# Kernel optimization log

Measured on AMD Instinct MI355X. Metric: run time of the kernel, lower is better.

Reference implementation:

```python
import jax, jax.numpy as jnp
from jax import lax
import numpy as np


def conv2d(x, w, b=None, stride=1, padding=0, groups=1, dilation=1):
    out = lax.conv_general_dilated(
        x, w, (stride, stride), [(padding, padding)] * 2,
        rhs_dilation=(dilation, dilation), feature_group_count=groups,
        dimension_numbers=('NCHW', 'OIHW', 'NCHW'))
    return out if b is None else out + b[None, :, None, None]


def unfold1d(x, k, axis):
    # torch.nn.functional.unfold with kernel (k,1) or (1,k), pad k//2 on that axis.
    # Returns [B, C, k, H, W] (channel-major, kernel-tap inner), matching torch layout.
    pad = k // 2
    pads = [(0, 0)] * 4
    pads[axis] = (pad, pad)
    xp = jnp.pad(x, pads)
    return jnp.stack([lax.slice_in_dim(xp, i, i + x.shape[axis], axis=axis)
                      for i in range(k)], axis=2)


def ikba(x, att, k, g, b_cb, w_cb):
    # Per-pixel dynamic grouped conv: attention mixes nset codebook kernels,
    # applied as vertical (k,1) then horizontal (1,k) unfold-matmul-fold.
    B, c, H, W = x.shape
    nset = att.shape[1]
    cg = c // g
    P = H * W
    a = att.reshape(B, nset, P).transpose(0, 2, 1)          # [B,P,nset]
    bias = a @ b_cb[0]                                      # [B,P,c]
    attk = a @ w_cb[0]                                      # [B,P, 2*c*cg*k]
    half = attk.shape[-1] // 2
    ah = attk[..., :half].reshape(B, P, g, cg, cg * k)
    aw = attk[..., half:].reshape(B, P, g, cg, cg * k)
    # vertical pass
    ufh = unfold1d(x, k, 2).reshape(B, g, cg * k, P).transpose(0, 3, 1, 2)  # [B,P,g,cg*k]
    xh = jnp.einsum('bpgij,bpgj->bpgi', ah, ufh).reshape(B, P, c)
    xh = xh.transpose(0, 2, 1).reshape(B, c, H, W)
    # horizontal pass
    ufw = unfold1d(xh, k, 3).reshape(B, g, cg * k, P).transpose(0, 3, 1, 2)
    xw = jnp.einsum('bpgij,bpgj->bpgi', aw, ufw).reshape(B, P, c) + bias
    return xw.transpose(0, 2, 1).reshape(B, c, H, W)


def hff_forward(x, dw1_w, dw2_w, proj_w, lka0_w, lkas_w, lka1_w, lka1_b,
                sca_w, sca_b, c1a_w, c1b_w, c2a_w, c2a_b, c2b_w, c2b_b,
                c211_w, c211_b, w_cb, b_cb, attgamma, ga1):
    C = x.shape[1]
    K, GC = 3, 4
    g = C // GC
    sca = conv2d(jnp.mean(x, axis=(2, 3), keepdims=True), sca_w, sca_b)
    x1 = conv2d(conv2d(x, dw1_w), dw2_w, padding=1, groups=C)
    lka = conv2d(conv2d(conv2d(x, lka0_w, padding=2, groups=C),
                        lkas_w, padding=9, groups=C, dilation=3), lka1_w, lka1_b)
    t = conv2d(x, c2a_w, c2a_b, padding=1, groups=c2a_w.shape[0])
    t1, t2 = jnp.split(t, 2, axis=1)  # SimpleGate
    att = conv2d(t1 * t2, c2b_w, c2b_b) * attgamma + conv2d(x, c211_w, c211_b)
    uf = conv2d(conv2d(x, c1a_w), c1b_w, padding=1, groups=C)
    x2 = ikba(uf, att, K, g, b_cb, w_cb) * ga1 + uf
    return conv2d(x1 * x2 * sca * lka, proj_w)


def setup_inputs() -> dict:
    key = jax.random.key(0)
    ks = jax.random.split(key, 24)
    B, C, H, W = 2, 256, 64, 64
    nset, k, gc = 128, 3, 4
    g = C // gc
    cg = C // g
    def rn(i, shape, scale=0.02):
        return jax.random.normal(ks[i], shape, jnp.float32) * scale
    return {
        'x': jax.random.normal(ks[0], (B, C, H, W), jnp.float32),
        'dw1_w': rn(1, (C, C, 1, 1)),
        'dw2_w': rn(2, (C, 1, 3, 3), 0.1),
        'proj_w': rn(3, (C, C, 1, 1)),
        'lka0_w': rn(4, (C, 1, 5, 5), 0.1),
        'lkas_w': rn(5, (C, 1, 7, 7), 0.1),
        'lka1_w': rn(6, (C, C, 1, 1)),
        'lka1_b': rn(7, (C,)),
        'sca_w': rn(8, (C, C, 1, 1)),
        'sca_b': rn(9, (C,)),
        'c1a_w': rn(10, (C, C, 1, 1)),
        'c1b_w': rn(11, (C, 1, 3, 3), 0.1),
        'c2a_w': rn(12, (32, C // 32, 3, 3), 0.1),
        'c2a_b': rn(13, (32,)),
        'c2b_w': rn(14, (nset, 16, 1, 1), 0.1),
        'c2b_b': rn(15, (nset,)),
        'c211_w': rn(16, (nset, C, 1, 1)),
        'c211_b': rn(17, (nset,)),
        'w_cb': rn(18, (1, nset, C * cg * k * 2), 0.05),
        'b_cb': rn(19, (1, nset, C), 0.05),
        'attgamma': jnp.full((1, nset, 1, 1), 0.01, jnp.float32),
        'ga1': jnp.full((1, C, 1, 1), 0.01, jnp.float32),
    }


def reference(x, dw1_w, dw2_w, proj_w, lka0_w, lkas_w, lka1_w, lka1_b,
              sca_w, sca_b, c1a_w, c1b_w, c2a_w, c2a_b, c2b_w, c2b_b,
              c211_w, c211_b, w_cb, b_cb, attgamma, ga1):
    return hff_forward(x, dw1_w, dw2_w, proj_w, lka0_w, lkas_w, lka1_w, lka1_b,
                       sca_w, sca_b, c1a_w, c1b_w, c2a_w, c2a_b, c2b_w, c2b_b,
                       c211_w, c211_b, w_cb, b_cb, attgamma, ga1)
```

## Files before the change

### kernel.cpp

```cpp
#include <hip/hip_runtime.h>
#include <cstddef>

#define P_ 4096
#define HW_ 64

typedef __bf16 bf16x8 __attribute__((ext_vector_type(8)));
typedef float f32x4 __attribute__((ext_vector_type(4)));

__device__ inline ushort f2bf(float f) {
  unsigned u = __float_as_uint(f);
  unsigned r = (u + 0x7FFFu + ((u >> 16) & 1u)) >> 16;
  return (ushort)r;
}
__device__ inline float bf2f(ushort h) {
  return __uint_as_float(((unsigned)h) << 16);
}
__device__ inline unsigned pack2(ushort a, ushort b) {
  return (unsigned)a | ((unsigned)b << 16);
}


__device__ inline void xsplit_body(const float* sb, ushort* dhb, ushort* dlb,
                                   int p0, int K, char* smem) {
  float (*T)[65] = (float(*)[65])smem;
  int t = threadIdx.x;
#pragma unroll
  for (int i = 0; i < 32; ++i) {
    int l = i * 256 + t;
    int n = l >> 6, c = l & 63;
    T[n][c] = sb[(size_t)n * P_ + p0 + c];
  }
  __syncthreads();
#pragma unroll
  for (int i = 0; i < 4; ++i) {
    int l = i * 256 + t;
    int c = l >> 4, n8 = (l & 15) << 3;
    ushort vh[8], vl[8];
#pragma unroll
    for (int u = 0; u < 8; ++u) {
      float f = T[n8 + u][c];
      ushort h = f2bf(f);
      vh[u] = h;
      vl[u] = f2bf(f - bf2f(h));
    }
    *(uint4*)&dhb[(size_t)(p0 + c) * K + n8] = *(uint4*)vh;
    *(uint4*)&dlb[(size_t)(p0 + c) * K + n8] = *(uint4*)vl;
  }
}

__device__ inline void gemm_body(const ushort* Whb, const ushort* Wlb,
                                 const ushort* Xhb, const ushort* Xlb,
                                 const float* bias, float* out, int M, int m0,
                                 int p0, int b, int K, char* smem) {
  ushort* Wsh = (ushort*)smem;
  ushort* Wsl = (ushort*)(smem + 9216);
  ushort* Xsh = (ushort*)(smem + 18432);
  ushort* Xsl = (ushort*)(smem + 27648);
  int t = threadIdx.x;
  int w = t >> 6, lane = t & 63, lm = lane & 15, lq = lane >> 4;
  f32x4 C[4];
#pragma unroll
  for (int pt = 0; pt < 4; ++pt) C[pt] = (f32x4)(0.f);
  for (int k0 = 0; k0 < K; k0 += 64) {
#pragma unroll
    for (int i = 0; i < 2; ++i) {
      int u = i * 256 + t;
      int row = u >> 3, k8 = (u & 7) * 8;
      *(uint4*)&Wsh[row * 72 + k8] = *(const uint4*)&Whb[(size_t)row * K + k0 + k8];
      *(uint4*)&Wsl[row * 72 + k8] = *(const uint4*)&Wlb[(size_t)row * K + k0 + k8];
      *(uint4*)&Xsh[row * 72 + k8] = *(const uint4*)&Xhb[(size_t)row * K + k0 + k8];
      *(uint4*)&Xsl[row * 72 + k8] = *(const uint4*)&Xlb[(size_t)row * K + k0 + k8];
    }
    __syncthreads();
#pragma unroll
    for (int kt = 0; kt < 2; ++kt) {
      bf16x8 Ah = *(const bf16x8*)&Wsh[(w * 16 + lm) * 72 + kt * 32 + lq * 8];
      bf16x8 Al = *(const bf16x8*)&Wsl[(w * 16 + lm) * 72 + kt * 32 + lq * 8];
#pragma unroll
      for (int pt = 0; pt < 4; ++pt) {
        bf16x8 Bh = *(const bf16x8*)&Xsh[(pt * 16 + lm) * 72 + kt * 32 + lq * 8];
        bf16x8 Bl = *(const bf16x8*)&Xsl[(pt * 16 + lm) * 72 + kt * 32 + lq * 8];
        C[pt] = __builtin_amdgcn_mfma_f32_16x16x32_bf16(Ah, Bh, C[pt], 0, 0, 0);
        C[pt] = __builtin_amdgcn_mfma_f32_16x16x32_bf16(Al, Bh, C[pt], 0, 0, 0);
        C[pt] = __builtin_amdgcn_mfma_f32_16x16x32_bf16(Ah, Bl, C[pt], 0, 0, 0);
      }
    }
    __syncthreads();
  }
#pragma unroll
  for (int pt = 0; pt < 4; ++pt) {
    int p = p0 + pt * 16 + lm;
#pragma unroll
    for (int r = 0; r < 4; ++r) {
      int m = m0 + w * 16 + lq * 4 + r;
      float v = C[pt][r];
      if (bias) v += bias[m];
      out[((size_t)b * M + m) * P_ + p] = v;
    }
  }
}

__global__ __launch_bounds__(256) void prep_kernel(
    const float* __restrict__ w_cb, const float* __restrict__ dw1_w,
    const float* __restrict__ lka1_w, const float* __restrict__ c1a_w,
    const float* __restrict__ proj_w, const float* __restrict__ c211_w,
    const float* __restrict__ b_cb, ushort* __restrict__ wT,
    ushort* __restrict__ W5h, ushort* __restrict__ W5l,
    ushort* __restrict__ bth, ushort* __restrict__ btl,
    const float* __restrict__ x, float* __restrict__ mean,
    ushort* __restrict__ XTxh, ushort* __restrict__ XTxl,
    const float* __restrict__ w0, const float* __restrict__ w1,
    float* __restrict__ outlka) {
  __shared__ __align__(16) char smem[48448];
  float (*T)[65] = (float(*)[65])smem;
  int blk = blockIdx.x;
  int t = threadIdx.x;
  if (blk < 512) {
    float* p0a = (float*)smem;
    float* p1a = (float*)(smem + 19584);
    int bc = blk;
    const float* ib = x + (size_t)bc * P_;
    const float* wp0 = w0 + (size_t)(bc & 255) * 25;
    const float* wp1 = w1 + (size_t)(bc & 255) * 49;
    for (int i = t; i < 4896; i += 256) p0a[i] = 0.f;
    for (int i = t; i < 7216; i += 256) p1a[i] = 0.f;
    __syncthreads();
#pragma unroll
    for (int i = 0; i < 4; ++i) {
      int l = i * 1024 + t * 4;
      int y = l >> 6, xx = l & 63;
      *(float4*)&p0a[(y + 2) * 72 + 4 + xx] = *(const float4*)(ib + l);
    }
    __syncthreads();
    int x0 = (t & 15) * 4, y0 = (t >> 4) * 4;
    {
      float acc[4][4] = {};
#pragma unroll
      for (int ry = 0; ry < 8; ++ry) {
        const float* row = &p0a[(y0 + ry) * 72 + x0];
        float4 v0 = *(const float4*)row;
        float4 v1 = *(const float4*)(row + 4);
        float4 v2 = *(const float4*)(row + 8);
        float rv[12] = {v0.x, v0.y, v0.z, v0.w, v1.x, v1.y, v1.z, v1.w,
                        v2.x, v2.y, v2.z, v2.w};
#pragma unroll
        for (int oy = 0; oy < 4; ++oy) {
          int dy = ry - oy;
          if (dy >= 0 && dy <= 4) {
#pragma unroll
            for (int dx = 0; dx < 5; ++dx) {
              float wv = wp0[dy * 5 + dx];
#pragma unroll
              for (int ox = 0; ox < 4; ++ox)
                acc[oy][ox] += wv * rv[2 + ox + dx];
            }
          }
        }
      }
#pragma unroll
      for (int oy = 0; oy < 4; ++oy) {
        float4 v = {acc[oy][0], acc[oy][1], acc[oy][2], acc[oy][3]};
        *(float4*)&p1a[(y0 + oy + 9) * 88 + 12 + x0] = v;
      }
    }
    __syncthreads();
    {
      float acc[4][4] = {};
#pragma unroll
      for (int ry = 0; ry < 22; ++ry) {
        const float* row = &p1a[(y0 + ry) * 88 + x0];
        float rv[28];
#pragma unroll
        for (int q = 0; q < 7; ++q)
          *(float4*)&rv[q * 4] = *(const float4*)(row + q * 4);
#pragma unroll
        for (int oy = 0; oy < 4; ++oy) {
          int d = ry - oy;
          if (d >= 0 && d <= 18 && (d % 3) == 0) {
            int dy = d / 3;
#pragma unroll
            for (int dx = 0; dx < 7; ++dx) {
              float wv = wp1[dy * 7 + dx];
#pragma unroll
              for (int ox = 0; ox < 4; ++ox)
                acc[oy][ox] += wv * rv[3 + ox + 3 * dx];
            }
          }
        }
      }
      float* ob = outlka + (size_t)bc * P_;
#pragma unroll
      for (int oy = 0; oy < 4; ++oy) {
        float4 v = {acc[oy][0], acc[oy][1], acc[oy][2], acc[oy][3]};
        *(float4*)&ob[(y0 + oy) * 64 + x0] = v;
      }
    }
  } else if (blk < 608) {
    int c0 = (blk - 512) * 64;
#pragma unroll
    for (int i = 0; i < 32; ++i) {
      int l = i * 256 + t;
      int n = l >> 6, c = l & 63;
      T[n][c] = w_cb[(size_t)n * 6144 + c0 + c];
    }
    __syncthreads();
#pragma unroll
    for (int i = 0; i < 4; ++i) {
      int l = i * 256 + t;
      int c = l >> 4, n8 = (l & 15) << 3;
      ushort v[8];
#pragma unroll
      for (int u = 0; u < 8; ++u) v[u] = f2bf(T[n8 + u][c]);
      *(uint4*)&wT[(size_t)(c0 + c) * 128 + n8] = *(uint4*)v;
    }
  } else if (blk < 752) {
    int f = (blk - 608) * 2048 + t * 8;
    const float* srcs[5] = {dw1_w, lka1_w, c1a_w, proj_w, c211_w};
    const int base[6] = {0, 65536, 131072, 196608, 262144, 294912};
    int r = 0;
    while (f >= base[r + 1]) ++r;
    const float* s = srcs[r] + (f - base[r]);
    float4 a = *(const float4*)s;
    float4 b4 = *(const float4*)(s + 4);
    float vv[8] = {a.x, a.y, a.z, a.w, b4.x, b4.y, b4.z, b4.w};
    ushort vh[8], vl[8];
#pragma unroll
    for (int u = 0; u < 8; ++u) {
      ushort h = f2bf(vv[u]);
      vh[u] = h;
      vl[u] = f2bf(vv[u] - bf2f(h));
    }
    *(uint4*)&W5h[f] = *(uint4*)vh;
    *(uint4*)&W5l[f] = *(uint4*)vl;
  } else if (blk < 756) {
    int c0 = (blk - 752) * 64;
#pragma unroll
    for (int i = 0; i < 32; ++i) {
      int l = i * 256 + t;
      int n = l >> 6, c = l & 63;
      T[n][c] = b_cb[(size_t)n * 256 + c0 + c];
    }
    __syncthreads();
#pragma unroll
    for (int i = 0; i < 4; ++i) {
      int l = i * 256 + t;
      int c = l >> 4, n8 = (l & 15) << 3;
      ushort vh[8], vl[8];
#pragma unroll
      for (int u = 0; u < 8; ++u) {
        float fv = T[n8 + u][c];
        ushort h = f2bf(fv);
        vh[u] = h;
        vl[u] = f2bf(fv - bf2f(h));
      }
      *(uint4*)&bth[(size_t)(c0 + c) * 128 + n8] = *(uint4*)vh;
      *(uint4*)&btl[(size_t)(c0 + c) * 128 + n8] = *(uint4*)vl;
    }
  } else if (blk < 1268) {
    int bc = blk - 756;
    const float* xp = x + (size_t)bc * P_;
    float s = 0.f;
    for (int i = t; i < P_; i += 256) s += xp[i];
    float* red = (float*)smem;
    red[t] = s;
    __syncthreads();
    for (int off2 = 128; off2 > 0; off2 >>= 1) {
      if (t < off2) red[t] += red[t + off2];
      __syncthreads();
    }
    if (t == 0) mean[bc] = red[0] * (1.f / P_);
  } else {
    const int K = 256;
    int l = blk - 1268;
    int p0 = (l & 63) * 64;
    int kb = (l >> 6) & 1;
    int b = l >> 7;
    xsplit_body(x + ((size_t)b * K + kb * 128) * P_,
                XTxh + (size_t)b * P_ * K + (size_t)kb * 128,
                XTxl + (size_t)b * P_ * K + (size_t)kb * 128, p0, K, smem);
  }
}

__global__ __launch_bounds__(256) void main1_kernel(
    const ushort* __restrict__ Xh, const ushort* __restrict__ Xl,
    const ushort* __restrict__ W5h, const ushort* __restrict__ W5l,
    const float* __restrict__ c211_b, float* __restrict__ dw1_out,
    float* __restrict__ B3, float* __restrict__ att0,
    const float* __restrict__ x, const float* __restrict__ c2aw,
    const float* __restrict__ c2ab, float* __restrict__ sgate,
    const float* __restrict__ B6, ushort* __restrict__ XT2h,
    ushort* __restrict__ XT2l, const float* __restrict__ mean,
    const float* __restrict__ sca_w, const float* __restrict__ sca_b,
    float* __restrict__ sca) {
  __shared__ __align__(16) char smem[36864];
  int blk = blockIdx.x;
  int t = threadIdx.x;
  if (blk < 1280) {
    const int K = 256;
    int p = blk & 63;
    int my = (blk >> 6) % 10;
    int b = blk / 640;
    const ushort *Wh, *Wl;
    float* out;
    const float* bias = nullptr;
    int M, m0;
    if (my < 4) {
      Wh = W5h; Wl = W5l; out = dw1_out; M = 256; m0 = my * 64;
    } else if (my < 8) {
      Wh = W5h + 131072; Wl = W5l + 131072; out = B3; M = 256; m0 = (my - 4) * 64;
    } else {
      Wh = W5h + 262144; Wl = W5l + 262144; out = att0; M = 128;
      m0 = (my - 8) * 64; bias = c211_b;
    }
    int p0 = p * 64;
    gemm_body(Wh + (size_t)m0 * K, Wl + (size_t)m0 * K,
              Xh + ((size_t)b * P_ + p0) * K, Xl + ((size_t)b * P_ + p0) * K,
              bias, out, M, m0, p0, b, K, smem);
  } else if (blk < 1792) {
    int idx = (blk - 1280) * 256 + t;
    int xq = idx & 63, y = (idx >> 6) & 63, go = (idx >> 12) & 15, b = idx >> 16;
    float acc[2];
#pragma unroll
    for (int h = 0; h < 2; ++h) {
      int gc = go + h * 16;
      const float* wr = c2aw + gc * 72;
      const float* xb = x + ((size_t)b * 256 + gc * 8) * P_;
      float ss = c2ab[gc];
      for (int ci = 0; ci < 8; ++ci)
        for (int dy = 0; dy < 3; ++dy) {
          int yy = y + dy - 1;
          if (yy < 0 || yy >= 64) continue;
          for (int dx = 0; dx < 3; ++dx) {
            int xx = xq + dx - 1;
            if (xx < 0 || xx >= 64) continue;
            ss += wr[ci * 9 + dy * 3 + dx] * xb[(size_t)ci * P_ + yy * 64 + xx];
          }
        }
      acc[h] = ss;
    }
    sgate[idx] = acc[0] * acc[1];
  } else if (blk < 2048) {
    const int K = 256;
    int l = blk - 1792;
    int p0 = (l & 63) * 64;
    int kb = (l >> 6) & 1;
    int b = l >> 7;
    xsplit_body(B6 + ((size_t)b * K + kb * 128) * P_,
                XT2h + (size_t)b * P_ * K + (size_t)kb * 128,
                XT2l + (size_t)b * P_ * K + (size_t)kb * 128, p0, K, smem);
  } else {
    int b = blk - 2048, c = t;
    const float* mb = mean + b * 256;
    const float* wr = sca_w + c * 256;
    float s = sca_b[c];
    for (int k = 0; k < 256; ++k) s += wr[k] * mb[k];
    sca[b * 256 + c] = s;
  }
}

__global__ __launch_bounds__(256) void k3_kernel(
    const ushort* __restrict__ Wh, const ushort* __restrict__ Wl,
    const ushort* __restrict__ XT2h, const ushort* __restrict__ XT2l,
    const float* __restrict__ lka1_b, float* __restrict__ B1,
    const float* __restrict__ sb, const float* __restrict__ c2bw,
    const float* __restrict__ c2bb, const float* __restrict__ gamma,
    const float* __restrict__ res, ushort* __restrict__ outh,
    ushort* __restrict__ outl, const float* __restrict__ in1,
    const float* __restrict__ w1, float* __restrict__ out1,
    const float* __restrict__ in2, const float* __restrict__ w2,
    float* __restrict__ out2) {
  __shared__ __align__(16) char smem[36864];
  int blk = blockIdx.x;
  int t = threadIdx.x;
  if (blk < 512) {
    const int K = 256;
    int p0 = (blk & 63) * 64;
    int m0 = ((blk >> 6) & 3) * 64;
    int b = blk >> 8;
    gemm_body(Wh + (size_t)m0 * K, Wl + (size_t)m0 * K,
              XT2h + ((size_t)b * P_ + p0) * K, XT2l + ((size_t)b * P_ + p0) * K,
              lka1_b, B1, 256, m0, p0, b, K, smem);
  } else if (blk < 768) {
    const int K = 16, M = 128;
    int l = blk - 512;
    int p0 = (l & 63) * 64;
    int m0 = ((l >> 6) & 1) * 64;
    int b = l >> 7;
    float (*Ws)[68] = (float(*)[68])smem;
    float (*Xs)[68] = (float(*)[68])(smem + 4352 * 4);
    int tm = t >> 4, tp = t & 15;
    float acc[4][4] = {};
    const float* inb = sb + (size_t)b * K * P_;
    {
      int kk = t >> 4, pq = (t & 15) << 2;
      float4 v = *(const float4*)(inb + (size_t)kk * P_ + p0 + pq);
      *(float4*)&Xs[kk][pq] = v;
    }
    {
      int mm = t >> 2, kq = (t & 3) << 2;
      float4 v = *(const float4*)(c2bw + (size_t)(m0 + mm) * K + kq);
      Ws[kq + 0][mm] = v.x; Ws[kq + 1][mm] = v.y;
      Ws[kq + 2][mm] = v.z; Ws[kq + 3][mm] = v.w;
    }
    __syncthreads();
#pragma unroll
    for (int kk = 0; kk < 16; ++kk) {
      const float4 wv = *(const float4*)&Ws[kk][tm << 2];
      const float4 xv = *(const float4*)&Xs[kk][tp << 2];
      const float wa[4] = {wv.x, wv.y, wv.z, wv.w};
      const float xa[4] = {xv.x, xv.y, xv.z, xv.w};
#pragma unroll
      for (int i = 0; i < 4; ++i)
#pragma unroll
        for (int j = 0; j < 4; ++j) acc[i][j] += wa[i] * xa[j];
    }
    float val[4][4];
#pragma unroll
    for (int i = 0; i < 4; ++i) {
      int m = m0 + (tm << 2) + i;
      float bv = c2bb[m], gm = gamma[m];
      float4 rv = *(const float4*)(res + ((size_t)b * M + m) * P_ + p0 + (tp << 2));
      val[i][0] = (acc[i][0] + bv) * gm + rv.x;
      val[i][1] = (acc[i][1] + bv) * gm + rv.y;
      val[i][2] = (acc[i][2] + bv) * gm + rv.z;
      val[i][3] = (acc[i][3] + bv) * gm + rv.w;
    }
#pragma unroll
    for (int j = 0; j < 4; ++j) {
      int p = p0 + (tp << 2) + j;
      ushort vh[4], vl[4];
#pragma unroll
      for (int i = 0; i < 4; ++i) {
        float f = val[i][j];
        ushort h = f2bf(f);
        vh[i] = h;
        vl[i] = f2bf(f - bf2f(h));
      }
      size_t a = ((size_t)b * P_ + p) * 128 + m0 + (tm << 2);
      uint2 hv, lv;
      hv.x = pack2(vh[0], vh[1]); hv.y = pack2(vh[2], vh[3]);
      lv.x = pack2(vl[0], vl[1]); lv.y = pack2(vl[2], vl[3]);
      *(uint2*)&outh[a] = hv;
      *(uint2*)&outl[a] = lv;
    }
  } else {
    float* pl = (float*)smem;
    int l = blk - 768;
    int which = l >> 9;
    int bc = l & 511;
    const float* in = which ? in2 : in1;
    const float* w = which ? w2 : w1;
    float* out = which ? out2 : out1;
    const float* ib = in + (size_t)bc * P_;
    const float* wp = w + (size_t)(bc & 255) * 9;
    for (int i = t; i < 4752; i += 256) pl[i] = 0.f;
    __syncthreads();
#pragma unroll
    for (int i = 0; i < 4; ++i) {
      int ll = i * 1024 + t * 4;
      int y = ll >> 6, xx = ll & 63;
      *(float4*)&pl[(y + 1) * 72 + 4 + xx] = *(const float4*)(ib + ll);
    }
    __syncthreads();
    int x0 = (t & 15) * 4, y0 = (t >> 4) * 4;
    float acc[4][4] = {};
#pragma unroll
    for (int ry = 0; ry < 6; ++ry) {
      const float* row = &pl[(y0 + ry) * 72 + x0];
      float4 v0 = *(const float4*)row;
      float4 v1 = *(const float4*)(row + 4);
      float4 v2 = *(const float4*)(row + 8);
      float rv[12] = {v0.x, v0.y, v0.z, v0.w, v1.x, v1.y, v1.z, v1.w,
                      v2.x, v2.y, v2.z, v2.w};
#pragma unroll
      for (int oy = 0; oy < 4; ++oy) {
        int dy = ry - oy;
        if (dy >= 0 && dy <= 2) {
#pragma unroll
          for (int dx = 0; dx < 3; ++dx) {
            float wv = wp[dy * 3 + dx];
#pragma unroll
            for (int ox = 0; ox < 4; ++ox)
              acc[oy][ox] += wv * rv[3 + ox + dx];
          }
        }
      }
    }
    float* ob = out + (size_t)bc * P_;
#pragma unroll
    for (int oy = 0; oy < 4; ++oy) {
      float4 v = {acc[oy][0], acc[oy][1], acc[oy][2], acc[oy][3]};
      *(float4*)&ob[(y0 + oy) * 64 + x0] = v;
    }
  }
}

__global__ __launch_bounds__(256) void ikba_mfma_kernel(
    const float* __restrict__ in, const ushort* __restrict__ attT,
    const ushort* __restrict__ Wt, int dirH, int wofs,
    const ushort* __restrict__ bth, const ushort* __restrict__ btl,
    const float* __restrict__ uf_ep, const float* __restrict__ ga1,
    const float* __restrict__ x1, const float* __restrict__ lka,
    const float* __restrict__ sca, ushort* __restrict__ pXh,
    ushort* __restrict__ pXl, float* __restrict__ outV) {
  __shared__ float Ts[4][64][17];

  int t = threadIdx.x;
  int b = blockIdx.z;
  int quad = blockIdx.y;
  int y = blockIdx.x;
  int p0 = y * 64;
  int gg = t >> 6;
  int lane = t & 63;
  int lm = lane & 15, lq = lane >> 4;
  int gi = quad * 4 + gg;
  int x = lane;
  float (*Tsw)[17] = Ts[gg];

  const ushort* Wbase = Wt + ((size_t)wofs + (size_t)gi * 48) * 128;
  bf16x8 Af[3][4];
#pragma unroll
  for (int ct = 0; ct < 3; ++ct)
#pragma unroll
    for (int K = 0; K < 4; ++K)
      Af[ct][K] = *(const bf16x8*)&Wbase[(ct * 16 + lm) * 128 + K * 32 + lq * 8];

  const ushort* Ab = attT + ((size_t)b * P_ + p0) * 128;
  f32x4 Cf[3][4];
#pragma unroll
  for (int ct = 0; ct < 3; ++ct)
#pragma unroll
    for (int pt = 0; pt < 4; ++pt) Cf[ct][pt] = (f32x4)(0.f);

#pragma unroll
  for (int pt = 0; pt < 4; ++pt) {
    bf16x8 Bf[4];
#pragma unroll
    for (int K = 0; K < 4; ++K)
      Bf[K] = *(const bf16x8*)&Ab[(pt * 16 + lm) * 128 + K * 32 + lq * 8];
#pragma unroll
    for (int ct = 0; ct < 3; ++ct)
#pragma unroll
      for (int K = 0; K < 4; ++K)
        Cf[ct][pt] = __builtin_amdgcn_mfma_f32_16x16x32_bf16(
            Af[ct][K], Bf[K], Cf[ct][pt], 0, 0, 0);
  }

  float u[12];
  const float* inb = in + ((size_t)b * 256 + gi * 4) * P_;
  if (dirH) {
#pragma unroll
    for (int j = 0; j < 12; ++j) {
      int ci = j / 3, tap = j % 3;
      int xx = x + tap - 1;
      u[j] = (xx >= 0 && xx < 64) ? inb[(size_t)ci * P_ + p0 + xx] : 0.f;
    }
  } else {
#pragma unroll
    for (int j = 0; j < 12; ++j) {
      int ci = j / 3, tap = j % 3;
      int yy = y + tap - 1;
      u[j] = (yy >= 0 && yy < 64) ? inb[(size_t)ci * P_ + yy * 64 + x] : 0.f;
    }
  }

  float s4[4] = {0.f, 0.f, 0.f, 0.f};
#pragma unroll
  for (int ct = 0; ct < 3; ++ct) {
#pragma unroll
    for (int pt = 0; pt < 4; ++pt)
#pragma unroll
      for (int r = 0; r < 4; ++r)
        Tsw[pt * 16 + lm][lq * 4 + r] = Cf[ct][pt][r];
    float tv[16];
#pragma unroll
    for (int c4 = 0; c4 < 4; ++c4)
      *(float4*)&tv[c4 * 4] = *(const float4*)&Tsw[x][c4 * 4];
#pragma unroll
    for (int c = 0; c < 16; ++c) {
      int col = ct * 16 + c;
      int i = col / 12, j = col % 12;
      s4[i] += tv[c] * u[j];
    }
  }

  if (dirH) {
    bf16x8 Abh[4], Abl[4];
#pragma unroll
    for (int K = 0; K < 4; ++K) {
      Abh[K] = *(const bf16x8*)&bth[(size_t)(quad * 16 + lm) * 128 + K * 32 + lq * 8];
      Abl[K] = *(const bf16x8*)&btl[(size_t)(quad * 16 + lm) * 128 + K * 32 + lq * 8];
    }
#pragma unroll
    for (int pt = 0; pt < 4; ++pt) {
      f32x4 Cb = (f32x4)(0.f);
#pragma unroll
      for (int K = 0; K < 4; ++K) {
        bf16x8 Bb = *(const bf16x8*)&Ab[(pt * 16 + lm) * 128 + K * 32 + lq * 8];
        Cb = __builtin_amdgcn_mfma_f32_16x16x32_bf16(Abh[K], Bb, Cb, 0, 0, 0);
        Cb = __builtin_amdgcn_mfma_f32_16x16x32_bf16(Abl[K], Bb, Cb, 0, 0, 0);
      }
#pragma unroll
      for (int r = 0; r < 4; ++r)
        Tsw[pt * 16 + lm][lq * 4 + r] = Cb[r];
    }
    float4 bl4 = *(const float4*)&Tsw[x][gg * 4];
    const float blv[4] = {bl4.x, bl4.y, bl4.z, bl4.w};
    ushort vh[4], vl[4];
#pragma unroll
    for (int i = 0; i < 4; ++i) {
      int ch = gi * 4 + i;
      size_t oidx = ((size_t)b * 256 + ch) * P_ + p0 + x;
      float x2v = (s4[i] + blv[i]) * ga1[ch] + uf_ep[oidx];
      float pr = x1[oidx] * x2v * sca[b * 256 + ch] * lka[oidx];
      ushort h = f2bf(pr);
      vh[i] = h;
      vl[i] = f2bf(pr - bf2f(h));
    }
    size_t xa = ((size_t)b * P_ + p0 + x) * 256 + quad * 16 + gg * 4;
    uint2 hv, lv;
    hv.x = pack2(vh[0], vh[1]); hv.y = pack2(vh[2], vh[3]);
    lv.x = pack2(vl[0], vl[1]); lv.y = pack2(vl[2], vl[3]);
    *(uint2*)&pXh[xa] = hv;
    *(uint2*)&pXl[xa] = lv;
  } else {
#pragma unroll
    for (int i = 0; i < 4; ++i) {
      int ch = gi * 4 + i;
      outV[((size_t)b * 256 + ch) * P_ + p0 + x] = s4[i];
    }
  }
}

__global__ __launch_bounds__(256) void gemm_bf16s_kernel(
    const ushort* __restrict__ Wh, const ushort* __restrict__ Wl,
    const ushort* __restrict__ Xh, const ushort* __restrict__ Xl,
    const float* __restrict__ bias, float* __restrict__ out, int M, int K) {
  __shared__ __align__(16) char smem[36864];
  int p0 = blockIdx.x * 64, m0 = blockIdx.y * 64, b = blockIdx.z;
  gemm_body(Wh + (size_t)m0 * K, Wl + (size_t)m0 * K,
            Xh + ((size_t)b * P_ + p0) * K, Xl + ((size_t)b * P_ + p0) * K,
            bias, out, M, m0, p0, b, K, smem);
}

extern "C" void kernel_launch(void* const* d_in, const int* in_sizes, int n_in,
                              void* d_out, int out_size, void* d_ws, size_t ws_size,
                              hipStream_t stream) {
  const float* x      = (const float*)d_in[0];
  const float* dw1_w  = (const float*)d_in[1];
  const float* dw2_w  = (const float*)d_in[2];
  const float* proj_w = (const float*)d_in[3];
  const float* lka0_w = (const float*)d_in[4];
  const float* lkas_w = (const float*)d_in[5];
  const float* lka1_w = (const float*)d_in[6];
  const float* lka1_b = (const float*)d_in[7];
  const float* sca_w  = (const float*)d_in[8];
  const float* sca_b  = (const float*)d_in[9];
  const float* c1a_w  = (const float*)d_in[10];
  const float* c1b_w  = (const float*)d_in[11];
  const float* c2a_w  = (const float*)d_in[12];
  const float* c2a_b  = (const float*)d_in[13];
  const float* c2b_w  = (const float*)d_in[14];
  const float* c2b_b  = (const float*)d_in[15];
  const float* c211_w = (const float*)d_in[16];
  const float* c211_b = (const float*)d_in[17];
  const float* w_cb   = (const float*)d_in[18];
  const float* b_cb   = (const float*)d_in[19];
  const float* attg   = (const float*)d_in[20];
  const float* ga1    = (const float*)d_in[21];
  float* out = (float*)d_out;

  const size_t NCHW = 2u * 256u * P_;
  float* ws = (float*)d_ws;
  size_t off = 0;
  float* meanb = ws + off; off += 512;
  float* scab  = ws + off; off += 512;
  float* B1 = ws + off; off += NCHW;
  float* B2 = ws + off; off += NCHW;
  float* B3 = ws + off; off += NCHW;
  float* B4 = ws + off; off += NCHW;
  float* B5 = ws + off; off += NCHW;
  float* B6 = ws + off; off += NCHW;
  float* sb   = ws + off; off += 2u * 16u * P_;
  float* att0 = ws + off; off += 2u * 128u * P_;
  ushort* wT    = (ushort*)(ws + off); off += 393216;
  ushort* W5h   = (ushort*)(ws + off); off += 147456;
  ushort* W5l   = (ushort*)(ws + off); off += 147456;
  ushort* bth   = (ushort*)(ws + off); off += 16384;
  ushort* btl   = (ushort*)(ws + off); off += 16384;
  ushort* XTxh  = (ushort*)(ws + off); off += 1048576;
  ushort* XTxl  = (ushort*)(ws + off); off += 1048576;
  ushort* XT2h  = (ushort*)(ws + off); off += 1048576;
  ushort* XT2l  = (ushort*)(ws + off); off += 1048576;
  ushort* XT3h  = (ushort*)(ws + off); off += 1048576;
  ushort* XT3l  = (ushort*)(ws + off); off += 1048576;
  ushort* attTh = (ushort*)(ws + off); off += 524288;
  ushort* attTl = (ushort*)(ws + off); off += 524288;

  const ushort* Wlka1h = W5h + 65536,  *Wlka1l = W5l + 65536;
  const ushort* Wprojh = W5h + 196608, *Wprojl = W5l + 196608;

  dim3 blk(256);

  prep_kernel<<<1524, blk, 0, stream>>>(w_cb, dw1_w, lka1_w, c1a_w, proj_w,
                                        c211_w, b_cb, wT, W5h, W5l, bth, btl,
                                        x, meanb, XTxh, XTxl,
                                        lka0_w, lkas_w, B6);
  main1_kernel<<<2050, blk, 0, stream>>>(XTxh, XTxl, W5h, W5l, c211_b,
                                         B4, B3, att0, x, c2a_w, c2a_b, sb,
                                         B6, XT2h, XT2l, meanb, sca_w, sca_b,
                                         scab);
  k3_kernel<<<1792, blk, 0, stream>>>(Wlka1h, Wlka1l, XT2h, XT2l, lka1_b, B1,
                                      sb, c2b_w, c2b_b, attg, att0,
                                      attTh, attTl,
                                      B4, dw2_w, B2, B3, c1b_w, B5);
  dim3 gik(64, 16, 2);
  ikba_mfma_kernel<<<gik, blk, 0, stream>>>(B5, attTh, wT, 0, 0, nullptr, nullptr,
                                            nullptr, nullptr, nullptr, nullptr,
                                            nullptr, nullptr, nullptr, B6);
  ikba_mfma_kernel<<<gik, blk, 0, stream>>>(B6, attTh, wT, 1, 3072, bth, btl,
                                            B5, ga1, B2, B1, scab, XT3h, XT3l,
                                            nullptr);
  gemm_bf16s_kernel<<<dim3(64, 4, 2), blk, 0, stream>>>(Wprojh, Wprojl, XT3h,
                                                        XT3l, nullptr, out, 256, 256);
}
```

Measured before the change: 274.3 us.

## Fuse vertical and horizontal IKBA passes into one kernel via shared-memory row

The vertical and horizontal dynamic-conv passes now run in a single kernel. Each block computes the vertical result for one image row and keeps it in shared memory with zero halo, and the horizontal pass reads its three taps from there. This removes one kernel launch and the global write and re-read of the intermediate B6. The centre tap of the unfold input is reused for the residual term, and the attention B-fragments are shared between the horizontal weight MFMA and the bias MFMA. In exchange, register and LDS pressure per block go up.

```diff
diff --git a/kernel.cpp b/kernel.cpp
--- a/kernel.cpp
+++ b/kernel.cpp
@@ -495,115 +495,162 @@
   }
 }
 
-__global__ __launch_bounds__(256) void ikba_mfma_kernel(
-    const float* __restrict__ in, const ushort* __restrict__ attT,
-    const ushort* __restrict__ Wt, int dirH, int wofs,
-    const ushort* __restrict__ bth, const ushort* __restrict__ btl,
-    const float* __restrict__ uf_ep, const float* __restrict__ ga1,
+__global__ __launch_bounds__(256) void ikba_fused_kernel(
+    const float* __restrict__ uf, const ushort* __restrict__ attT,
+    const ushort* __restrict__ Wt, const ushort* __restrict__ bth,
+    const ushort* __restrict__ btl, const float* __restrict__ ga1,
     const float* __restrict__ x1, const float* __restrict__ lka,
     const float* __restrict__ sca, ushort* __restrict__ pXh,
-    ushort* __restrict__ pXl, float* __restrict__ outV) {
+    ushort* __restrict__ pXl) {
   __shared__ float Ts[4][64][17];
+  __shared__ float XH[4][4][68];
 
   int t = threadIdx.x;
-  int b = blockIdx.z;
-  int quad = blockIdx.y;
-  int y = blockIdx.x;
+  int b = blockIdx.z, quad = blockIdx.y, y = blockIdx.x;
   int p0 = y * 64;
-  int gg = t >> 6;
-  int lane = t & 63;
+  int gg = t >> 6, lane = t & 63;
   int lm = lane & 15, lq = lane >> 4;
   int gi = quad * 4 + gg;
   int x = lane;
   float (*Tsw)[17] = Ts[gg];
-
-  const ushort* Wbase = Wt + ((size_t)wofs + (size_t)gi * 48) * 128;
-  bf16x8 Af[3][4];
-#pragma unroll
-  for (int ct = 0; ct < 3; ++ct)
-#pragma unroll
-    for (int K = 0; K < 4; ++K)
-      Af[ct][K] = *(const bf16x8*)&Wbase[(ct * 16 + lm) * 128 + K * 32 + lq * 8];
+  float (*XHw)[68] = XH[gg];
 
   const ushort* Ab = attT + ((size_t)b * P_ + p0) * 128;
-  f32x4 Cf[3][4];
-#pragma unroll
-  for (int ct = 0; ct < 3; ++ct)
-#pragma unroll
-    for (int pt = 0; pt < 4; ++pt) Cf[ct][pt] = (f32x4)(0.f);
-
-#pragma unroll
-  for (int pt = 0; pt < 4; ++pt) {
-    bf16x8 Bf[4];
-#pragma unroll
-    for (int K = 0; K < 4; ++K)
-      Bf[K] = *(const bf16x8*)&Ab[(pt * 16 + lm) * 128 + K * 32 + lq * 8];
+  const float* ufb = uf + ((size_t)b * 256 + gi * 4) * P_;
+  float uf_mid[4];
+
+  {
+    const ushort* Wbase = Wt + (size_t)gi * 48 * 128;
+    bf16x8 Af[3][4];
 #pragma unroll
     for (int ct = 0; ct < 3; ++ct)
 #pragma unroll
       for (int K = 0; K < 4; ++K)
-        Cf[ct][pt] = __builtin_amdgcn_mfma_f32_16x16x32_bf16(
-            Af[ct][K], Bf[K], Cf[ct][pt], 0, 0, 0);
-  }
-
-  float u[12];
-  const float* inb = in + ((size_t)b * 256 + gi * 4) * P_;
-  if (dirH) {
-#pragma unroll
-    for (int j = 0; j < 12; ++j) {
-      int ci = j / 3, tap = j % 3;
-      int xx = x + tap - 1;
-      u[j] = (xx >= 0 && xx < 64) ? inb[(size_t)ci * P_ + p0 + xx] : 0.f;
-    }
-  } else {
+        Af[ct][K] = *(const bf16x8*)&Wbase[(ct * 16 + lm) * 128 + K * 32 + lq * 8];
+    f32x4 Cf[3][4];
+#pragma unroll
+    for (int ct = 0; ct < 3; ++ct)
+#pragma unroll
+      for (int pt = 0; pt < 4; ++pt) Cf[ct][pt] = (f32x4)(0.f);
+#pragma unroll
+    for (int pt = 0; pt < 4; ++pt) {
+      bf16x8 Bf[4];
+#pragma unroll
+      for (int K = 0; K < 4; ++K)
+        Bf[K] = *(const bf16x8*)&Ab[(pt * 16 + lm) * 128 + K * 32 + lq * 8];
+#pragma unroll
+      for (int ct = 0; ct < 3; ++ct)
+#pragma unroll
+        for (int K = 0; K < 4; ++K)
+          Cf[ct][pt] = __builtin_amdgcn_mfma_f32_16x16x32_bf16(
+              Af[ct][K], Bf[K], Cf[ct][pt], 0, 0, 0);
+    }
+    float u[12];
 #pragma unroll
     for (int j = 0; j < 12; ++j) {
       int ci = j / 3, tap = j % 3;
       int yy = y + tap - 1;
-      u[j] = (yy >= 0 && yy < 64) ? inb[(size_t)ci * P_ + yy * 64 + x] : 0.f;
-    }
-  }
-
-  float s4[4] = {0.f, 0.f, 0.f, 0.f};
-#pragma unroll
-  for (int ct = 0; ct < 3; ++ct) {
-#pragma unroll
-    for (int pt = 0; pt < 4; ++pt)
-#pragma unroll
-      for (int r = 0; r < 4; ++r)
-        Tsw[pt * 16 + lm][lq * 4 + r] = Cf[ct][pt][r];
-    float tv[16];
-#pragma unroll
-    for (int c4 = 0; c4 < 4; ++c4)
-      *(float4*)&tv[c4 * 4] = *(const float4*)&Tsw[x][c4 * 4];
-#pragma unroll
-    for (int c = 0; c < 16; ++c) {
-      int col = ct * 16 + c;
-      int i = col / 12, j = col % 12;
-      s4[i] += tv[c] * u[j];
-    }
-  }
-
-  if (dirH) {
+      u[j] = (yy >= 0 && yy < 64) ? ufb[(size_t)ci * P_ + yy * 64 + x] : 0.f;
+    }
+#pragma unroll
+    for (int ci = 0; ci < 4; ++ci) uf_mid[ci] = u[ci * 3 + 1];
+    float s4[4] = {0.f, 0.f, 0.f, 0.f};
+#pragma unroll
+    for (int ct = 0; ct < 3; ++ct) {
+#pragma unroll
+      for (int pt = 0; pt < 4; ++pt)
+#pragma unroll
+        for (int r = 0; r < 4; ++r)
+          Tsw[pt * 16 + lm][lq * 4 + r] = Cf[ct][pt][r];
+      float tv[16];
+#pragma unroll
+      for (int c4 = 0; c4 < 4; ++c4)
+        *(float4*)&tv[c4 * 4] = *(const float4*)&Tsw[x][c4 * 4];
+#pragma unroll
+      for (int c = 0; c < 16; ++c) {
+        int col = ct * 16 + c;
+        int i = col / 12, j = col % 12;
+        s4[i] += tv[c] * u[j];
+      }
+    }
+    if (lane < 2) {
+#pragma unroll
+      for (int ci = 0; ci < 4; ++ci) XHw[ci][lane * 65] = 0.f;
+    }
+#pragma unroll
+    for (int ci = 0; ci < 4; ++ci) XHw[ci][x + 1] = s4[ci];
+  }
+
+  {
+    const ushort* Wbase = Wt + ((size_t)3072 + (size_t)gi * 48) * 128;
+    bf16x8 Af[3][4];
+#pragma unroll
+    for (int ct = 0; ct < 3; ++ct)
+#pragma unroll
+      for (int K = 0; K < 4; ++K)
+        Af[ct][K] = *(const bf16x8*)&Wbase[(ct * 16 + lm) * 128 + K * 32 + lq * 8];
     bf16x8 Abh[4], Abl[4];
 #pragma unroll
     for (int K = 0; K < 4; ++K) {
       Abh[K] = *(const bf16x8*)&bth[(size_t)(quad * 16 + lm) * 128 + K * 32 + lq * 8];
       Abl[K] = *(const bf16x8*)&btl[(size_t)(quad * 16 + lm) * 128 + K * 32 + lq * 8];
     }
+    f32x4 Ch[3][4];
+#pragma unroll
+    for (int ct = 0; ct < 3; ++ct)
+#pragma unroll
+      for (int pt = 0; pt < 4; ++pt) Ch[ct][pt] = (f32x4)(0.f);
+    f32x4 Cb[4];
+#pragma unroll
+    for (int pt = 0; pt < 4; ++pt) Cb[pt] = (f32x4)(0.f);
 #pragma unroll
     for (int pt = 0; pt < 4; ++pt) {
-      f32x4 Cb = (f32x4)(0.f);
+      bf16x8 Bf[4];
+#pragma unroll
+      for (int K = 0; K < 4; ++K)
+        Bf[K] = *(const bf16x8*)&Ab[(pt * 16 + lm) * 128 + K * 32 + lq * 8];
+#pragma unroll
+      for (int ct = 0; ct < 3; ++ct)
+#pragma unroll
+        for (int K = 0; K < 4; ++K)
+          Ch[ct][pt] = __builtin_amdgcn_mfma_f32_16x16x32_bf16(
+              Af[ct][K], Bf[K], Ch[ct][pt], 0, 0, 0);
 #pragma unroll
       for (int K = 0; K < 4; ++K) {
-        bf16x8 Bb = *(const bf16x8*)&Ab[(pt * 16 + lm) * 128 + K * 32 + lq * 8];
-        Cb = __builtin_amdgcn_mfma_f32_16x16x32_bf16(Abh[K], Bb, Cb, 0, 0, 0);
-        Cb = __builtin_amdgcn_mfma_f32_16x16x32_bf16(Abl[K], Bb, Cb, 0, 0, 0);
-      }
+        Cb[pt] = __builtin_amdgcn_mfma_f32_16x16x32_bf16(Abh[K], Bf[K], Cb[pt], 0, 0, 0);
+        Cb[pt] = __builtin_amdgcn_mfma_f32_16x16x32_bf16(Abl[K], Bf[K], Cb[pt], 0, 0, 0);
+      }
+    }
+    float u[12];
+#pragma unroll
+    for (int j = 0; j < 12; ++j) {
+      int ci = j / 3, tap = j % 3;
+      u[j] = XHw[ci][x + tap];
+    }
+    float s4[4] = {0.f, 0.f, 0.f, 0.f};
+#pragma unroll
+    for (int ct = 0; ct < 3; ++ct) {
+#pragma unroll
+      for (int pt = 0; pt < 4; ++pt)
+#pragma unroll
+        for (int r = 0; r < 4; ++r)
+          Tsw[pt * 16 + lm][lq * 4 + r] = Ch[ct][pt][r];
+      float tv[16];
+#pragma unroll
+      for (int c4 = 0; c4 < 4; ++c4)
+        *(float4*)&tv[c4 * 4] = *(const float4*)&Tsw[x][c4 * 4];
+#pragma unroll
+      for (int c = 0; c < 16; ++c) {
+        int col = ct * 16 + c;
+        int i = col / 12, j = col % 12;
+        s4[i] += tv[c] * u[j];
+      }
+    }
+#pragma unroll
+    for (int pt = 0; pt < 4; ++pt)
 #pragma unroll
       for (int r = 0; r < 4; ++r)
-        Tsw[pt * 16 + lm][lq * 4 + r] = Cb[r];
-    }
+        Tsw[pt * 16 + lm][lq * 4 + r] = Cb[pt][r];
     float4 bl4 = *(const float4*)&Tsw[x][gg * 4];
     const float blv[4] = {bl4.x, bl4.y, bl4.z, bl4.w};
     ushort vh[4], vl[4];
@@ -611,7 +658,7 @@
     for (int i = 0; i < 4; ++i) {
       int ch = gi * 4 + i;
       size_t oidx = ((size_t)b * 256 + ch) * P_ + p0 + x;
-      float x2v = (s4[i] + blv[i]) * ga1[ch] + uf_ep[oidx];
+      float x2v = (s4[i] + blv[i]) * ga1[ch] + uf_mid[i];
       float pr = x1[oidx] * x2v * sca[b * 256 + ch] * lka[oidx];
       ushort h = f2bf(pr);
       vh[i] = h;
@@ -623,12 +670,6 @@
     lv.x = pack2(vl[0], vl[1]); lv.y = pack2(vl[2], vl[3]);
     *(uint2*)&pXh[xa] = hv;
     *(uint2*)&pXl[xa] = lv;
-  } else {
-#pragma unroll
-    for (int i = 0; i < 4; ++i) {
-      int ch = gi * 4 + i;
-      outV[((size_t)b * 256 + ch) * P_ + p0 + x] = s4[i];
-    }
   }
 }
 
@@ -715,12 +756,8 @@
                                       attTh, attTl,
                                       B4, dw2_w, B2, B3, c1b_w, B5);
   dim3 gik(64, 16, 2);
-  ikba_mfma_kernel<<<gik, blk, 0, stream>>>(B5, attTh, wT, 0, 0, nullptr, nullptr,
-                                            nullptr, nullptr, nullptr, nullptr,
-                                            nullptr, nullptr, nullptr, B6);
-  ikba_mfma_kernel<<<gik, blk, 0, stream>>>(B6, attTh, wT, 1, 3072, bth, btl,
-                                            B5, ga1, B2, B1, scab, XT3h, XT3l,
-                                            nullptr);
+  ikba_fused_kernel<<<gik, blk, 0, stream>>>(B5, attTh, wT, bth, btl, ga1,
+                                             B2, B1, scab, XT3h, XT3l);
   gemm_bf16s_kernel<<<dim3(64, 4, 2), blk, 0, stream>>>(Wprojh, Wprojl, XT3h,
                                                         XT3l, nullptr, out, 256, 256);
 }
```

After: 251.7 us. 1.09x faster.
